# Kernel tuning notes

Measured on AMD Instinct MI355X. Metric: run time of the kernel, lower is better.

Reference implementation:

```python
import jax, jax.numpy as jnp
import numpy as np

BS, N, C_IMG, C_PT, H, W = 8, 100000, 512, 256, 48, 160


def setup_inputs() -> dict:
    key = jax.random.key(0)
    ks = jax.random.split(key, 8)
    point_feat = jax.random.normal(ks[0], (N, C_PT), dtype=jnp.float32)
    # pillar centers in LiDAR frame: x forward [10,60], y left [-10,10], z [-2,1]
    u = jax.random.uniform(ks[1], (N, 3), dtype=jnp.float32)
    pillar_centers = jnp.stack([
        10.0 + 50.0 * u[:, 0],
        -10.0 + 20.0 * u[:, 1],
        -2.0 + 3.0 * u[:, 2],
    ], axis=1)
    batch_idx = jax.random.randint(ks[2], (N,), 0, BS, dtype=jnp.int32)
    img_feat = jax.random.normal(ks[3], (BS, C_IMG, H, W), dtype=jnp.float32)
    # KITTI-style calibration (per batch, small jitter)
    f, cx, cy = 80.0, 80.0, 24.0
    P2_base = np.array([[f, 0, cx, 0], [0, f, cy, 0], [0, 0, 1, 0]], dtype=np.float32)
    Tr_base = np.array([[0, -1, 0, 0], [0, 0, -1, 0], [1, 0, 0, 0], [0, 0, 0, 1]], dtype=np.float32)
    rng = np.random.RandomState(0)
    P2 = np.stack([P2_base + 0.01 * rng.randn(3, 4).astype(np.float32) for _ in range(BS)])
    R0 = np.stack([np.eye(4, dtype=np.float32) for _ in range(BS)])
    Tr = np.stack([Tr_base + 0.001 * rng.randn(4, 4).astype(np.float32) for _ in range(BS)])
    align_w = jax.random.normal(ks[4], (C_PT, C_IMG), dtype=jnp.float32) * 0.02
    align_b = jax.random.normal(ks[5], (C_PT,), dtype=jnp.float32) * 0.02
    return {
        'point_feat': point_feat, 'pillar_centers': pillar_centers,
        'img_feat': img_feat, 'P2': jnp.asarray(P2), 'R0': jnp.asarray(R0),
        'Tr': jnp.asarray(Tr), 'align_w': align_w, 'align_b': align_b,
        'batch_idx': batch_idx, 'img_h': H, 'img_w': W,
    }


def _fuse(point_feat, pillar_centers, img_feat, P2, R0, Tr, align_w, align_b,
          batch_idx, img_h, img_w):
    n = point_feat.shape[0]
    dt = point_feat.dtype
    # --- project_to_image (vectorized over all points via per-point calib gather) ---
    pts_hom = jnp.concatenate([pillar_centers, jnp.ones((n, 1), dtype=dt)], axis=1)  # [N,4]
    pts_cam = jnp.einsum('nij,nj->ni', Tr[batch_idx], pts_hom)    # [N,4]
    pts_rect = jnp.einsum('nij,nj->ni', R0[batch_idx], pts_cam)   # [N,4]
    pts_img = jnp.einsum('nij,nj->ni', P2[batch_idx], pts_rect)   # [N,3]
    depth = jnp.clip(pts_img[:, 2:3], 1e-5, None)
    uv = pts_img[:, :2] / depth
    valid = ((pts_img[:, 2] > 0) & (uv[:, 0] >= 0) & (uv[:, 0] < img_w)
             & (uv[:, 1] >= 0) & (uv[:, 1] < img_h))
    # --- grid_sample bilinear, align_corners=True, padding_mode='zeros' ---
    # grid = 2*uv/(dim-1)-1 with align_corners=True => pixel coords == uv.
    _, C, Hf, Wf = img_feat.shape
    u_, v_ = uv[:, 0], uv[:, 1]
    x0 = jnp.floor(u_); y0 = jnp.floor(v_)
    wx1 = u_ - x0; wx0 = 1.0 - wx1
    wy1 = v_ - y0; wy0 = 1.0 - wy1

    def gather(xi, yi):
        inb = (xi >= 0) & (xi <= Wf - 1) & (yi >= 0) & (yi <= Hf - 1)
        xc = jnp.clip(xi, 0, Wf - 1).astype(jnp.int32)
        yc = jnp.clip(yi, 0, Hf - 1).astype(jnp.int32)
        f = img_feat[batch_idx, :, yc, xc]  # [N,C]
        return f * inb.astype(dt)[:, None]

    sampled = (gather(x0, y0) * (wx0 * wy0)[:, None]
               + gather(x0 + 1, y0) * (wx1 * wy0)[:, None]
               + gather(x0, y0 + 1) * (wx0 * wy1)[:, None]
               + gather(x0 + 1, y0 + 1) * (wx1 * wy1)[:, None])
    sampled = jnp.where(valid[:, None], sampled, jnp.zeros((), dtype=dt))
    # --- align (Linear) + residual add ---
    aligned = sampled @ align_w.T + align_b
    return point_feat + aligned


def reference(point_feat, pillar_centers, img_feat, P2, R0, Tr, align_w, align_b,
              batch_idx, img_h, img_w):
    return _fuse(point_feat, pillar_centers, img_feat, P2, R0, Tr,
                 align_w, align_b, batch_idx, img_h, img_w)
```

## Files before the change

### kernel.cpp

```cpp
#include <hip/hip_runtime.h>

#define C_IMG 512
#define C_PT  256
#define IMG_H 48
#define IMG_W 160
#define HWPIX (IMG_H * IMG_W)

#define MP   64
#define BK   64
#define SPAD 72

typedef short bf16x8 __attribute__((ext_vector_type(8)));
typedef float f32x4  __attribute__((ext_vector_type(4)));

static __device__ __forceinline__ unsigned short f2bf(float f) {
    unsigned u = __float_as_uint(f);
    u += 0x7fffu + ((u >> 16) & 1u);
    return (unsigned short)(u >> 16);
}
static __device__ __forceinline__ unsigned pack2(float lo, float hi) {
    return (unsigned)f2bf(lo) | ((unsigned)f2bf(hi) << 16);
}
static __device__ __forceinline__ float bflo(unsigned v) { return __uint_as_float(v << 16); }
static __device__ __forceinline__ float bfhi(unsigned v) { return __uint_as_float(v & 0xffff0000u); }

__global__ __launch_bounds__(256)
void transpose_kernel(const float* __restrict__ img, unsigned short* __restrict__ imgT) {
    __shared__ float tile[64][33];
    const int b   = blockIdx.z;
    const int hw0 = blockIdx.x * 32;
    const int c0  = blockIdx.y * 64;
    const int tx  = threadIdx.x;
    const int ty  = threadIdx.y;
    const float* src = img + (size_t)b * C_IMG * HWPIX;
    #pragma unroll
    for (int i = 0; i < 64; i += 8)
        tile[ty + i][tx] = src[(size_t)(c0 + ty + i) * HWPIX + hw0 + tx];
    __syncthreads();
    unsigned* dst = (unsigned*)(imgT + (size_t)b * HWPIX * C_IMG);
    #pragma unroll
    for (int i = 0; i < 32; i += 8) {
        const int hw = ty + i;
        dst[(size_t)(hw0 + hw) * (C_IMG / 2) + (c0 >> 1) + tx] =
            pack2(tile[2 * tx][hw], tile[2 * tx + 1][hw]);
    }
}

__global__ __launch_bounds__(256)
void cvt_w_kernel(const float* __restrict__ alw, unsigned short* __restrict__ alwT) {
    const int i = (blockIdx.x * 256 + threadIdx.x) * 8;
    const float4 a = *(const float4*)(alw + i);
    const float4 b = *(const float4*)(alw + i + 4);
    uint4 o;
    o.x = pack2(a.x, a.y); o.y = pack2(a.z, a.w);
    o.z = pack2(b.x, b.y); o.w = pack2(b.z, b.w);
    *(uint4*)(alwT + i) = o;
}

static __device__ __forceinline__ void gather_issue(
    const unsigned short* __restrict__ ib, const int* co, int cb, uint4* g)
{
    #pragma unroll
    for (int c = 0; c < 4; ++c) {
        g[2 * c]     = *(const uint4*)(ib + co[c] + cb);
        g[2 * c + 1] = *(const uint4*)(ib + co[c] + cb + 8);
    }
}
static __device__ __forceinline__ void gather_commit(
    unsigned short* __restrict__ dst, const uint4* g, const float* cw)
{
    #pragma unroll
    for (int h = 0; h < 2; ++h) {
        const unsigned* u0 = (const unsigned*)&g[0 + h];
        const unsigned* u1 = (const unsigned*)&g[2 + h];
        const unsigned* u2 = (const unsigned*)&g[4 + h];
        const unsigned* u3 = (const unsigned*)&g[6 + h];
        uint4 ov; unsigned* op = (unsigned*)&ov;
        #pragma unroll
        for (int wI = 0; wI < 4; ++wI) {
            const float vlo = cw[0]*bflo(u0[wI]) + cw[1]*bflo(u1[wI])
                            + cw[2]*bflo(u2[wI]) + cw[3]*bflo(u3[wI]);
            const float vhi = cw[0]*bfhi(u0[wI]) + cw[1]*bfhi(u1[wI])
                            + cw[2]*bfhi(u2[wI]) + cw[3]*bfhi(u3[wI]);
            op[wI] = pack2(vlo, vhi);
        }
        *(uint4*)(dst + h * 8) = ov;
    }
}

__global__ __launch_bounds__(256, 3)
void fused_trans_kernel(const float* __restrict__ pf,
                        const float* __restrict__ centers,
                        const unsigned short* __restrict__ imgT,
                        const unsigned short* __restrict__ alwT,
                        const float* __restrict__ P2,
                        const float* __restrict__ R0,
                        const float* __restrict__ Tr,
                        const float* __restrict__ alb,
                        const int*   __restrict__ bidx,
                        float* __restrict__ out,
                        int n)
{
    __shared__ float          sWg[MP][4];
    __shared__ int            sOf[MP][4];
    __shared__ unsigned short sS[2][MP][SPAD];

    const int tid = threadIdx.x;
    const int pt0 = blockIdx.x * MP;

    if (tid < MP) {
        const int p = pt0 + tid;
        float w[4] = {0.f, 0.f, 0.f, 0.f};
        int   o[4] = {0, 0, 0, 0};
        if (p < n) {
            const float cx = centers[p * 3 + 0];
            const float cy = centers[p * 3 + 1];
            const float cz = centers[p * 3 + 2];
            const int   b  = bidx[p];
            const float* tr = Tr + b * 16;
            const float c0 = tr[0]*cx + tr[1]*cy + tr[2]*cz + tr[3];
            const float c1 = tr[4]*cx + tr[5]*cy + tr[6]*cz + tr[7];
            const float c2 = tr[8]*cx + tr[9]*cy + tr[10]*cz + tr[11];
            const float c3 = tr[12]*cx + tr[13]*cy + tr[14]*cz + tr[15];
            const float* r0 = R0 + b * 16;
            const float e0 = r0[0]*c0 + r0[1]*c1 + r0[2]*c2 + r0[3]*c3;
            const float e1 = r0[4]*c0 + r0[5]*c1 + r0[6]*c2 + r0[7]*c3;
            const float e2 = r0[8]*c0 + r0[9]*c1 + r0[10]*c2 + r0[11]*c3;
            const float e3 = r0[12]*c0 + r0[13]*c1 + r0[14]*c2 + r0[15]*c3;
            const float* p2 = P2 + b * 12;
            const float ix = p2[0]*e0 + p2[1]*e1 + p2[2]*e2  + p2[3]*e3;
            const float iy = p2[4]*e0 + p2[5]*e1 + p2[6]*e2  + p2[7]*e3;
            const float iz = p2[8]*e0 + p2[9]*e1 + p2[10]*e2 + p2[11]*e3;
            const float depth = fmaxf(iz, 1e-5f);
            const float u = ix / depth;
            const float v = iy / depth;
            const bool valid = (iz > 0.f) && (u >= 0.f) && (u < (float)IMG_W)
                                         && (v >= 0.f) && (v < (float)IMG_H);
            const float x0f = floorf(u), y0f = floorf(v);
            const float wx1 = u - x0f, wx0 = 1.f - wx1;
            const float wy1 = v - y0f, wy0 = 1.f - wy1;
            const float cwv[4] = {wx0 * wy0, wx1 * wy0, wx0 * wy1, wx1 * wy1};
            #pragma unroll
            for (int j = 0; j < 4; ++j) {
                const float xf = x0f + (float)(j & 1);
                const float yf = y0f + (float)(j >> 1);
                const bool inb = (xf >= 0.f) && (xf <= (float)(IMG_W - 1))
                              && (yf >= 0.f) && (yf <= (float)(IMG_H - 1));
                const int xc = (int)fminf(fmaxf(xf, 0.f), (float)(IMG_W - 1));
                const int yc = (int)fminf(fmaxf(yf, 0.f), (float)(IMG_H - 1));
                w[j] = (valid && inb) ? cwv[j] : 0.f;
                o[j] = ((b * IMG_H + yc) * IMG_W + xc) * C_IMG;
            }
        }
        #pragma unroll
        for (int j = 0; j < 4; ++j) { sWg[tid][j] = w[j]; sOf[tid][j] = o[j]; }
    }

    f32x4 acc[4][4];
    #pragma unroll
    for (int i = 0; i < 4; ++i)
        #pragma unroll
        for (int j = 0; j < 4; ++j)
            acc[i][j] = (f32x4){0.f, 0.f, 0.f, 0.f};

    const int lane = tid & 63;
    const int wid  = tid >> 6;
    const int l15  = lane & 15;
    const int quad = lane >> 4;
    const int sp   = tid >> 2;
    const int ssub = tid & 3;

    __syncthreads();

    float cw[4]; int co[4];
    #pragma unroll
    for (int j = 0; j < 4; ++j) { cw[j] = sWg[sp][j]; co[j] = sOf[sp][j]; }
    const int cbase = ssub * 16;

    const unsigned short* bwp = alwT + (size_t)(wid * 64 + l15) * C_IMG + quad * 8;

    {
        uint4 g0[8];
        gather_issue(imgT, co, cbase, g0);
        gather_commit(&sS[0][sp][cbase], g0, cw);
    }
    __syncthreads();

    #pragma unroll
    for (int ck = 0; ck < C_IMG / BK; ++ck) {
        const int cur = ck & 1;
        uint4 gn[8];
        if (ck < C_IMG / BK - 1)
            gather_issue(imgT, co, (ck + 1) * BK + cbase, gn);

        #pragma unroll
        for (int kk = 0; kk < 2; ++kk) {
            bf16x8 bfr[4], af[4];
            #pragma unroll
            for (int nt = 0; nt < 4; ++nt)
                bfr[nt] = *(const bf16x8*)(bwp + nt * 16 * C_IMG + ck * BK + kk * 32);
            #pragma unroll
            for (int mt = 0; mt < 4; ++mt)
                af[mt] = *(const bf16x8*)&sS[cur][mt * 16 + l15][kk * 32 + quad * 8];
            #pragma unroll
            for (int mt = 0; mt < 4; ++mt)
                #pragma unroll
                for (int nt = 0; nt < 4; ++nt)
                    acc[mt][nt] = __builtin_amdgcn_mfma_f32_16x16x32_bf16(
                        af[mt], bfr[nt], acc[mt][nt], 0, 0, 0);
        }

        if (ck < C_IMG / BK - 1)
            gather_commit(&sS[cur ^ 1][sp][cbase], gn, cw);
        __syncthreads();
    }

    #pragma unroll
    for (int mt = 0; mt < 4; ++mt) {
        #pragma unroll
        for (int r = 0; r < 4; ++r) {
            const int p = pt0 + mt * 16 + quad * 4 + r;
            if (p < n) {
                #pragma unroll
                for (int nt = 0; nt < 4; ++nt) {
                    const int nc = wid * 64 + nt * 16 + l15;
                    const size_t idx = (size_t)p * C_PT + nc;
                    out[idx] = pf[idx] + alb[nc] + acc[mt][nt][r];
                }
            }
        }
    }
}

__global__ __launch_bounds__(256)
void fused_fallback_kernel(const float* __restrict__ pf,
                           const float* __restrict__ centers,
                           const float* __restrict__ img,
                           const float* __restrict__ P2,
                           const float* __restrict__ R0,
                           const float* __restrict__ Tr,
                           const float* __restrict__ alw,
                           const float* __restrict__ alb,
                           const int*   __restrict__ bidx,
                           float* __restrict__ out,
                           int n)
{
    __shared__ float          sWg[MP][4];
    __shared__ int            sOf[MP][4];
    __shared__ unsigned short sS[MP][SPAD];
    __shared__ unsigned short sW[C_PT][SPAD];

    const int tid = threadIdx.x;
    const int pt0 = blockIdx.x * MP;

    if (tid < MP) {
        const int p = pt0 + tid;
        float w[4] = {0.f, 0.f, 0.f, 0.f};
        int   o[4] = {0, 0, 0, 0};
        if (p < n) {
            const float cx = centers[p * 3 + 0];
            const float cy = centers[p * 3 + 1];
            const float cz = centers[p * 3 + 2];
            const int   b  = bidx[p];
            const float* tr = Tr + b * 16;
            const float c0 = tr[0]*cx + tr[1]*cy + tr[2]*cz + tr[3];
            const float c1 = tr[4]*cx + tr[5]*cy + tr[6]*cz + tr[7];
            const float c2 = tr[8]*cx + tr[9]*cy + tr[10]*cz + tr[11];
            const float c3 = tr[12]*cx + tr[13]*cy + tr[14]*cz + tr[15];
            const float* r0 = R0 + b * 16;
            const float e0 = r0[0]*c0 + r0[1]*c1 + r0[2]*c2 + r0[3]*c3;
            const float e1 = r0[4]*c0 + r0[5]*c1 + r0[6]*c2 + r0[7]*c3;
            const float e2 = r0[8]*c0 + r0[9]*c1 + r0[10]*c2 + r0[11]*c3;
            const float e3 = r0[12]*c0 + r0[13]*c1 + r0[14]*c2 + r0[15]*c3;
            const float* p2 = P2 + b * 12;
            const float ix = p2[0]*e0 + p2[1]*e1 + p2[2]*e2  + p2[3]*e3;
            const float iy = p2[4]*e0 + p2[5]*e1 + p2[6]*e2  + p2[7]*e3;
            const float iz = p2[8]*e0 + p2[9]*e1 + p2[10]*e2 + p2[11]*e3;
            const float depth = fmaxf(iz, 1e-5f);
            const float u = ix / depth;
            const float v = iy / depth;
            const bool valid = (iz > 0.f) && (u >= 0.f) && (u < (float)IMG_W)
                                         && (v >= 0.f) && (v < (float)IMG_H);
            const float x0f = floorf(u), y0f = floorf(v);
            const float wx1 = u - x0f, wx0 = 1.f - wx1;
            const float wy1 = v - y0f, wy0 = 1.f - wy1;
            const float cwv[4] = {wx0 * wy0, wx1 * wy0, wx0 * wy1, wx1 * wy1};
            #pragma unroll
            for (int j = 0; j < 4; ++j) {
                const float xf = x0f + (float)(j & 1);
                const float yf = y0f + (float)(j >> 1);
                const bool inb = (xf >= 0.f) && (xf <= (float)(IMG_W - 1))
                              && (yf >= 0.f) && (yf <= (float)(IMG_H - 1));
                const int xc = (int)fminf(fmaxf(xf, 0.f), (float)(IMG_W - 1));
                const int yc = (int)fminf(fmaxf(yf, 0.f), (float)(IMG_H - 1));
                w[j] = (valid && inb) ? cwv[j] : 0.f;
                o[j] = b * C_IMG * HWPIX + yc * IMG_W + xc;
            }
        }
        #pragma unroll
        for (int j = 0; j < 4; ++j) { sWg[tid][j] = w[j]; sOf[tid][j] = o[j]; }
    }

    f32x4 acc[4][4];
    #pragma unroll
    for (int i = 0; i < 4; ++i)
        #pragma unroll
        for (int j = 0; j < 4; ++j)
            acc[i][j] = (f32x4){0.f, 0.f, 0.f, 0.f};

    const int lane = tid & 63;
    const int wid  = tid >> 6;
    const int l15  = lane & 15;
    const int quad = lane >> 4;
    const int sp   = tid >> 2;
    const int ssub = tid & 3;

    __syncthreads();

    for (int ck = 0; ck < C_IMG / BK; ++ck) {
        {
            const float cw0 = sWg[sp][0], cw1 = sWg[sp][1], cw2 = sWg[sp][2], cw3 = sWg[sp][3];
            const int   co0 = sOf[sp][0], co1 = sOf[sp][1], co2 = sOf[sp][2], co3 = sOf[sp][3];
            const int   cb  = ck * BK + ssub * 16;
            const float* ib = img;
            #pragma unroll
            for (int h = 0; h < 2; ++h) {
                uint4 ov;
                unsigned* op = (unsigned*)&ov;
                #pragma unroll
                for (int wI = 0; wI < 4; ++wI) {
                    const int c = cb + h * 8 + 2 * wI;
                    const float vlo = cw0*ib[co0 + c*HWPIX] + cw1*ib[co1 + c*HWPIX]
                                    + cw2*ib[co2 + c*HWPIX] + cw3*ib[co3 + c*HWPIX];
                    const float vhi = cw0*ib[co0 + (c+1)*HWPIX] + cw1*ib[co1 + (c+1)*HWPIX]
                                    + cw2*ib[co2 + (c+1)*HWPIX] + cw3*ib[co3 + (c+1)*HWPIX];
                    op[wI] = pack2(vlo, vhi);
                }
                *(uint4*)&sS[sp][ssub * 16 + h * 8] = ov;
            }
        }
        {
            #pragma unroll
            for (int pass = 0; pass < 4; ++pass) {
                const int r = pass * 64 + (tid >> 2);
                const int c = (tid & 3) * 16;
                const float* wr = alw + (size_t)r * C_IMG + ck * BK + c;
                const float4 f0 = *(const float4*)(wr + 0);
                const float4 f1 = *(const float4*)(wr + 4);
                const float4 f2 = *(const float4*)(wr + 8);
                const float4 f3 = *(const float4*)(wr + 12);
                uint4 oa, ob;
                oa.x = pack2(f0.x, f0.y); oa.y = pack2(f0.z, f0.w);
                oa.z = pack2(f1.x, f1.y); oa.w = pack2(f1.z, f1.w);
                ob.x = pack2(f2.x, f2.y); ob.y = pack2(f2.z, f2.w);
                ob.z = pack2(f3.x, f3.y); ob.w = pack2(f3.z, f3.w);
                *(uint4*)&sW[r][c]     = oa;
                *(uint4*)&sW[r][c + 8] = ob;
            }
        }
        __syncthreads();

        #pragma unroll
        for (int kk = 0; kk < 2; ++kk) {
            bf16x8 af[4], bfr[4];
            #pragma unroll
            for (int mt = 0; mt < 4; ++mt)
                af[mt] = *(const bf16x8*)&sS[mt * 16 + l15][kk * 32 + quad * 8];
            #pragma unroll
            for (int nt = 0; nt < 4; ++nt)
                bfr[nt] = *(const bf16x8*)&sW[wid * 64 + nt * 16 + l15][kk * 32 + quad * 8];
            #pragma unroll
            for (int mt = 0; mt < 4; ++mt)
                #pragma unroll
                for (int nt = 0; nt < 4; ++nt)
                    acc[mt][nt] = __builtin_amdgcn_mfma_f32_16x16x32_bf16(
                        af[mt], bfr[nt], acc[mt][nt], 0, 0, 0);
        }
        __syncthreads();
    }

    #pragma unroll
    for (int mt = 0; mt < 4; ++mt) {
        #pragma unroll
        for (int r = 0; r < 4; ++r) {
            const int p = pt0 + mt * 16 + quad * 4 + r;
            if (p < n) {
                #pragma unroll
                for (int nt = 0; nt < 4; ++nt) {
                    const int nc = wid * 64 + nt * 16 + l15;
                    const size_t idx = (size_t)p * C_PT + nc;
                    out[idx] = pf[idx] + alb[nc] + acc[mt][nt][r];
                }
            }
        }
    }
}

extern "C" void kernel_launch(void* const* d_in, const int* in_sizes, int n_in,
                              void* d_out, int out_size, void* d_ws, size_t ws_size,
                              hipStream_t stream) {
    const float* pf      = (const float*)d_in[0];
    const float* centers = (const float*)d_in[1];
    const float* img     = (const float*)d_in[2];
    const float* P2      = (const float*)d_in[3];
    const float* R0      = (const float*)d_in[4];
    const float* Tr      = (const float*)d_in[5];
    const float* alw     = (const float*)d_in[6];
    const float* alb     = (const float*)d_in[7];
    const int*   bidx    = (const int*)d_in[8];
    float*       out     = (float*)d_out;

    const int n  = in_sizes[8];
    const int bs = in_sizes[3] / 12;
    const int nblk = (n + MP - 1) / MP;

    const size_t timg = (size_t)bs * HWPIX * C_IMG * sizeof(unsigned short);
    const size_t tw   = (size_t)C_PT * C_IMG * sizeof(unsigned short);
    if (ws_size >= timg + tw) {
        unsigned short* imgT = (unsigned short*)d_ws;
        unsigned short* alwT = (unsigned short*)((char*)d_ws + timg);
        transpose_kernel<<<dim3(HWPIX / 32, C_IMG / 64, bs), dim3(32, 8), 0, stream>>>(img, imgT);
        cvt_w_kernel<<<dim3((C_PT * C_IMG / 8) / 256), 256, 0, stream>>>(alw, alwT);
        fused_trans_kernel<<<nblk, 256, 0, stream>>>(
            pf, centers, imgT, alwT, P2, R0, Tr, alb, bidx, out, n);
    } else {
        fused_fallback_kernel<<<nblk, 256, 0, stream>>>(
            pf, centers, img, P2, R0, Tr, alw, alb, bidx, out, n);
    }
}
```

Baseline: 396.3 us.

## Project image features through linear layer before bilinear sampling

Bilinear interpolation and the linear align layer are both linear, so their order can be swapped. The weight matrix is now applied to every image pixel first (8*48*160 pixels instead of 100k points), giving a bf16 table with 256 channels per pixel. Each point then only gathers and blends four 256-channel rows and adds the residual and bias. This removes the per-point GEMM and the full-image transpose, at the cost of a dense per-pixel projection that reads the fp32 image with strided loads and writes a bf16 intermediate.

```diff
diff --git a/kernel.cpp b/kernel.cpp
--- a/kernel.cpp
+++ b/kernel.cpp
@@ -23,28 +23,6 @@
 }
 static __device__ __forceinline__ float bflo(unsigned v) { return __uint_as_float(v << 16); }
 static __device__ __forceinline__ float bfhi(unsigned v) { return __uint_as_float(v & 0xffff0000u); }
-
-__global__ __launch_bounds__(256)
-void transpose_kernel(const float* __restrict__ img, unsigned short* __restrict__ imgT) {
-    __shared__ float tile[64][33];
-    const int b   = blockIdx.z;
-    const int hw0 = blockIdx.x * 32;
-    const int c0  = blockIdx.y * 64;
-    const int tx  = threadIdx.x;
-    const int ty  = threadIdx.y;
-    const float* src = img + (size_t)b * C_IMG * HWPIX;
-    #pragma unroll
-    for (int i = 0; i < 64; i += 8)
-        tile[ty + i][tx] = src[(size_t)(c0 + ty + i) * HWPIX + hw0 + tx];
-    __syncthreads();
-    unsigned* dst = (unsigned*)(imgT + (size_t)b * HWPIX * C_IMG);
-    #pragma unroll
-    for (int i = 0; i < 32; i += 8) {
-        const int hw = ty + i;
-        dst[(size_t)(hw0 + hw) * (C_IMG / 2) + (c0 >> 1) + tx] =
-            pack2(tile[2 * tx][hw], tile[2 * tx + 1][hw]);
-    }
-}
 
 __global__ __launch_bounds__(256)
 void cvt_w_kernel(const float* __restrict__ alw, unsigned short* __restrict__ alwT) {
@@ -57,53 +35,178 @@
     *(uint4*)(alwT + i) = o;
 }
 
-static __device__ __forceinline__ void gather_issue(
-    const unsigned short* __restrict__ ib, const int* co, int cb, uint4* g)
+__global__ __launch_bounds__(256)
+void proj_kernel(const float* __restrict__ img,
+                 const unsigned short* __restrict__ wbf,
+                 unsigned short* __restrict__ PT) {
+    const int blk  = blockIdx.x;
+    const int b    = blk / (HWPIX / 64);
+    const int hw0  = (blk % (HWPIX / 64)) * 64;
+    const int tid  = threadIdx.x;
+    const int lane = tid & 63;
+    const int wid  = tid >> 6;
+    const int l15  = lane & 15;
+    const int quad = lane >> 4;
+
+    f32x4 acc[4][4];
+    #pragma unroll
+    for (int i = 0; i < 4; ++i)
+        #pragma unroll
+        for (int j = 0; j < 4; ++j)
+            acc[i][j] = (f32x4){0.f, 0.f, 0.f, 0.f};
+
+    const float* aim = img + (size_t)b * C_IMG * HWPIX + hw0 + l15;
+    const unsigned short* bw = wbf + (size_t)(wid * 64 + l15) * C_IMG + quad * 8;
+
+    for (int ck = 0; ck < C_IMG / 64; ++ck) {
+        #pragma unroll
+        for (int kk = 0; kk < 2; ++kk) {
+            const int c0 = ck * 64 + kk * 32 + quad * 8;
+            bf16x8 af[4];
+            #pragma unroll
+            for (int mt = 0; mt < 4; ++mt) {
+                const float* ap = aim + (size_t)c0 * HWPIX + mt * 16;
+                float f[8];
+                #pragma unroll
+                for (int j = 0; j < 8; ++j) f[j] = ap[j * HWPIX];
+                union { unsigned u[4]; bf16x8 v; } cv;
+                cv.u[0] = pack2(f[0], f[1]);
+                cv.u[1] = pack2(f[2], f[3]);
+                cv.u[2] = pack2(f[4], f[5]);
+                cv.u[3] = pack2(f[6], f[7]);
+                af[mt] = cv.v;
+            }
+            bf16x8 bfr[4];
+            #pragma unroll
+            for (int nt = 0; nt < 4; ++nt)
+                bfr[nt] = *(const bf16x8*)(bw + (size_t)(nt * 16) * C_IMG + ck * 64 + kk * 32);
+            #pragma unroll
+            for (int mt = 0; mt < 4; ++mt)
+                #pragma unroll
+                for (int nt = 0; nt < 4; ++nt)
+                    acc[mt][nt] = __builtin_amdgcn_mfma_f32_16x16x32_bf16(
+                        af[mt], bfr[nt], acc[mt][nt], 0, 0, 0);
+        }
+    }
+
+    #pragma unroll
+    for (int mt = 0; mt < 4; ++mt) {
+        #pragma unroll
+        for (int r = 0; r < 4; ++r) {
+            const int pix = mt * 16 + quad * 4 + r;
+            unsigned short* dst = PT + (size_t)(b * HWPIX + hw0 + pix) * C_PT;
+            #pragma unroll
+            for (int nt = 0; nt < 4; ++nt) {
+                const int nc = wid * 64 + nt * 16 + l15;
+                dst[nc] = f2bf(acc[mt][nt][r]);
+            }
+        }
+    }
+}
+
+#define PPW 4
+__global__ __launch_bounds__(256)
+void point_kernel(const float* __restrict__ pf,
+                  const float* __restrict__ centers,
+                  const unsigned short* __restrict__ PT,
+                  const float* __restrict__ P2,
+                  const float* __restrict__ R0,
+                  const float* __restrict__ Tr,
+                  const float* __restrict__ alb,
+                  const int*   __restrict__ bidx,
+                  float* __restrict__ out,
+                  int n)
 {
-    #pragma unroll
-    for (int c = 0; c < 4; ++c) {
-        g[2 * c]     = *(const uint4*)(ib + co[c] + cb);
-        g[2 * c + 1] = *(const uint4*)(ib + co[c] + cb + 8);
-    }
-}
-static __device__ __forceinline__ void gather_commit(
-    unsigned short* __restrict__ dst, const uint4* g, const float* cw)
-{
-    #pragma unroll
-    for (int h = 0; h < 2; ++h) {
-        const unsigned* u0 = (const unsigned*)&g[0 + h];
-        const unsigned* u1 = (const unsigned*)&g[2 + h];
-        const unsigned* u2 = (const unsigned*)&g[4 + h];
-        const unsigned* u3 = (const unsigned*)&g[6 + h];
-        uint4 ov; unsigned* op = (unsigned*)&ov;
-        #pragma unroll
-        for (int wI = 0; wI < 4; ++wI) {
-            const float vlo = cw[0]*bflo(u0[wI]) + cw[1]*bflo(u1[wI])
-                            + cw[2]*bflo(u2[wI]) + cw[3]*bflo(u3[wI]);
-            const float vhi = cw[0]*bfhi(u0[wI]) + cw[1]*bfhi(u1[wI])
-                            + cw[2]*bfhi(u2[wI]) + cw[3]*bfhi(u3[wI]);
-            op[wI] = pack2(vlo, vhi);
-        }
-        *(uint4*)(dst + h * 8) = ov;
-    }
-}
-
-__global__ __launch_bounds__(256, 3)
-void fused_trans_kernel(const float* __restrict__ pf,
-                        const float* __restrict__ centers,
-                        const unsigned short* __restrict__ imgT,
-                        const unsigned short* __restrict__ alwT,
-                        const float* __restrict__ P2,
-                        const float* __restrict__ R0,
-                        const float* __restrict__ Tr,
-                        const float* __restrict__ alb,
-                        const int*   __restrict__ bidx,
-                        float* __restrict__ out,
-                        int n)
+    const int tid  = threadIdx.x;
+    const int lane = tid & 63;
+    const int wid  = tid >> 6;
+    const int p0   = blockIdx.x * (4 * PPW) + wid * PPW;
+
+    const float4 ab = *(const float4*)(alb + lane * 4);
+
+    #pragma unroll
+    for (int it = 0; it < PPW; ++it) {
+        const int p = p0 + it;
+        if (p >= n) break;
+
+        const float cx = centers[p * 3 + 0];
+        const float cy = centers[p * 3 + 1];
+        const float cz = centers[p * 3 + 2];
+        const int   b  = bidx[p];
+        const float* tr = Tr + b * 16;
+        const float c0 = tr[0]*cx + tr[1]*cy + tr[2]*cz + tr[3];
+        const float c1 = tr[4]*cx + tr[5]*cy + tr[6]*cz + tr[7];
+        const float c2 = tr[8]*cx + tr[9]*cy + tr[10]*cz + tr[11];
+        const float c3 = tr[12]*cx + tr[13]*cy + tr[14]*cz + tr[15];
+        const float* r0 = R0 + b * 16;
+        const float e0 = r0[0]*c0 + r0[1]*c1 + r0[2]*c2 + r0[3]*c3;
+        const float e1 = r0[4]*c0 + r0[5]*c1 + r0[6]*c2 + r0[7]*c3;
+        const float e2 = r0[8]*c0 + r0[9]*c1 + r0[10]*c2 + r0[11]*c3;
+        const float e3 = r0[12]*c0 + r0[13]*c1 + r0[14]*c2 + r0[15]*c3;
+        const float* p2 = P2 + b * 12;
+        const float ix = p2[0]*e0 + p2[1]*e1 + p2[2]*e2  + p2[3]*e3;
+        const float iy = p2[4]*e0 + p2[5]*e1 + p2[6]*e2  + p2[7]*e3;
+        const float iz = p2[8]*e0 + p2[9]*e1 + p2[10]*e2 + p2[11]*e3;
+        const float depth = fmaxf(iz, 1e-5f);
+        const float u = ix / depth;
+        const float v = iy / depth;
+        const bool valid = (iz > 0.f) && (u >= 0.f) && (u < (float)IMG_W)
+                                     && (v >= 0.f) && (v < (float)IMG_H);
+        const float x0f = floorf(u), y0f = floorf(v);
+        const float wx1 = u - x0f, wx0 = 1.f - wx1;
+        const float wy1 = v - y0f, wy0 = 1.f - wy1;
+        const float cwv[4] = {wx0 * wy0, wx1 * wy0, wx0 * wy1, wx1 * wy1};
+        float wgt[4]; int off[4];
+        #pragma unroll
+        for (int j = 0; j < 4; ++j) {
+            const float xf = x0f + (float)(j & 1);
+            const float yf = y0f + (float)(j >> 1);
+            const bool inb = (xf >= 0.f) && (xf <= (float)(IMG_W - 1))
+                          && (yf >= 0.f) && (yf <= (float)(IMG_H - 1));
+            const int xc = (int)fminf(fmaxf(xf, 0.f), (float)(IMG_W - 1));
+            const int yc = (int)fminf(fmaxf(yf, 0.f), (float)(IMG_H - 1));
+            wgt[j] = (valid && inb) ? cwv[j] : 0.f;
+            off[j] = ((b * IMG_H + yc) * IMG_W + xc) * C_PT;
+        }
+
+        float s0 = 0.f, s1 = 0.f, s2 = 0.f, s3 = 0.f;
+        #pragma unroll
+        for (int j = 0; j < 4; ++j) {
+            const uint2 g = *(const uint2*)(PT + off[j] + lane * 4);
+            s0 = fmaf(wgt[j], bflo(g.x), s0);
+            s1 = fmaf(wgt[j], bfhi(g.x), s1);
+            s2 = fmaf(wgt[j], bflo(g.y), s2);
+            s3 = fmaf(wgt[j], bfhi(g.y), s3);
+        }
+
+        const size_t idx = (size_t)p * C_PT + lane * 4;
+        const float4 pv = *(const float4*)(pf + idx);
+        float4 ov;
+        ov.x = pv.x + ab.x + s0;
+        ov.y = pv.y + ab.y + s1;
+        ov.z = pv.z + ab.z + s2;
+        ov.w = pv.w + ab.w + s3;
+        *(float4*)(out + idx) = ov;
+    }
+}
+
+__global__ __launch_bounds__(256)
+void fused_fallback_kernel(const float* __restrict__ pf,
+                           const float* __restrict__ centers,
+                           const float* __restrict__ img,
+                           const float* __restrict__ P2,
+                           const float* __restrict__ R0,
+                           const float* __restrict__ Tr,
+                           const float* __restrict__ alw,
+                           const float* __restrict__ alb,
+                           const int*   __restrict__ bidx,
+                           float* __restrict__ out,
+                           int n)
 {
     __shared__ float          sWg[MP][4];
     __shared__ int            sOf[MP][4];
-    __shared__ unsigned short sS[2][MP][SPAD];
+    __shared__ unsigned short sS[MP][SPAD];
+    __shared__ unsigned short sW[C_PT][SPAD];
 
     const int tid = threadIdx.x;
     const int pt0 = blockIdx.x * MP;
@@ -149,151 +252,6 @@
                 const int xc = (int)fminf(fmaxf(xf, 0.f), (float)(IMG_W - 1));
                 const int yc = (int)fminf(fmaxf(yf, 0.f), (float)(IMG_H - 1));
                 w[j] = (valid && inb) ? cwv[j] : 0.f;
-                o[j] = ((b * IMG_H + yc) * IMG_W + xc) * C_IMG;
-            }
-        }
-        #pragma unroll
-        for (int j = 0; j < 4; ++j) { sWg[tid][j] = w[j]; sOf[tid][j] = o[j]; }
-    }
-
-    f32x4 acc[4][4];
-    #pragma unroll
-    for (int i = 0; i < 4; ++i)
-        #pragma unroll
-        for (int j = 0; j < 4; ++j)
-            acc[i][j] = (f32x4){0.f, 0.f, 0.f, 0.f};
-
-    const int lane = tid & 63;
-    const int wid  = tid >> 6;
-    const int l15  = lane & 15;
-    const int quad = lane >> 4;
-    const int sp   = tid >> 2;
-    const int ssub = tid & 3;
-
-    __syncthreads();
-
-    float cw[4]; int co[4];
-    #pragma unroll
-    for (int j = 0; j < 4; ++j) { cw[j] = sWg[sp][j]; co[j] = sOf[sp][j]; }
-    const int cbase = ssub * 16;
-
-    const unsigned short* bwp = alwT + (size_t)(wid * 64 + l15) * C_IMG + quad * 8;
-
-    {
-        uint4 g0[8];
-        gather_issue(imgT, co, cbase, g0);
-        gather_commit(&sS[0][sp][cbase], g0, cw);
-    }
-    __syncthreads();
-
-    #pragma unroll
-    for (int ck = 0; ck < C_IMG / BK; ++ck) {
-        const int cur = ck & 1;
-        uint4 gn[8];
-        if (ck < C_IMG / BK - 1)
-            gather_issue(imgT, co, (ck + 1) * BK + cbase, gn);
-
-        #pragma unroll
-        for (int kk = 0; kk < 2; ++kk) {
-            bf16x8 bfr[4], af[4];
-            #pragma unroll
-            for (int nt = 0; nt < 4; ++nt)
-                bfr[nt] = *(const bf16x8*)(bwp + nt * 16 * C_IMG + ck * BK + kk * 32);
-            #pragma unroll
-            for (int mt = 0; mt < 4; ++mt)
-                af[mt] = *(const bf16x8*)&sS[cur][mt * 16 + l15][kk * 32 + quad * 8];
-            #pragma unroll
-            for (int mt = 0; mt < 4; ++mt)
-                #pragma unroll
-                for (int nt = 0; nt < 4; ++nt)
-                    acc[mt][nt] = __builtin_amdgcn_mfma_f32_16x16x32_bf16(
-                        af[mt], bfr[nt], acc[mt][nt], 0, 0, 0);
-        }
-
-        if (ck < C_IMG / BK - 1)
-            gather_commit(&sS[cur ^ 1][sp][cbase], gn, cw);
-        __syncthreads();
-    }
-
-    #pragma unroll
-    for (int mt = 0; mt < 4; ++mt) {
-        #pragma unroll
-        for (int r = 0; r < 4; ++r) {
-            const int p = pt0 + mt * 16 + quad * 4 + r;
-            if (p < n) {
-                #pragma unroll
-                for (int nt = 0; nt < 4; ++nt) {
-                    const int nc = wid * 64 + nt * 16 + l15;
-                    const size_t idx = (size_t)p * C_PT + nc;
-                    out[idx] = pf[idx] + alb[nc] + acc[mt][nt][r];
-                }
-            }
-        }
-    }
-}
-
-__global__ __launch_bounds__(256)
-void fused_fallback_kernel(const float* __restrict__ pf,
-                           const float* __restrict__ centers,
-                           const float* __restrict__ img,
-                           const float* __restrict__ P2,
-                           const float* __restrict__ R0,
-                           const float* __restrict__ Tr,
-                           const float* __restrict__ alw,
-                           const float* __restrict__ alb,
-                           const int*   __restrict__ bidx,
-                           float* __restrict__ out,
-                           int n)
-{
-    __shared__ float          sWg[MP][4];
-    __shared__ int            sOf[MP][4];
-    __shared__ unsigned short sS[MP][SPAD];
-    __shared__ unsigned short sW[C_PT][SPAD];
-
-    const int tid = threadIdx.x;
-    const int pt0 = blockIdx.x * MP;
-
-    if (tid < MP) {
-        const int p = pt0 + tid;
-        float w[4] = {0.f, 0.f, 0.f, 0.f};
-        int   o[4] = {0, 0, 0, 0};
-        if (p < n) {
-            const float cx = centers[p * 3 + 0];
-            const float cy = centers[p * 3 + 1];
-            const float cz = centers[p * 3 + 2];
-            const int   b  = bidx[p];
-            const float* tr = Tr + b * 16;
-            const float c0 = tr[0]*cx + tr[1]*cy + tr[2]*cz + tr[3];
-            const float c1 = tr[4]*cx + tr[5]*cy + tr[6]*cz + tr[7];
-            const float c2 = tr[8]*cx + tr[9]*cy + tr[10]*cz + tr[11];
-            const float c3 = tr[12]*cx + tr[13]*cy + tr[14]*cz + tr[15];
-            const float* r0 = R0 + b * 16;
-            const float e0 = r0[0]*c0 + r0[1]*c1 + r0[2]*c2 + r0[3]*c3;
-            const float e1 = r0[4]*c0 + r0[5]*c1 + r0[6]*c2 + r0[7]*c3;
-            const float e2 = r0[8]*c0 + r0[9]*c1 + r0[10]*c2 + r0[11]*c3;
-            const float e3 = r0[12]*c0 + r0[13]*c1 + r0[14]*c2 + r0[15]*c3;
-            const float* p2 = P2 + b * 12;
-            const float ix = p2[0]*e0 + p2[1]*e1 + p2[2]*e2  + p2[3]*e3;
-            const float iy = p2[4]*e0 + p2[5]*e1 + p2[6]*e2  + p2[7]*e3;
-            const float iz = p2[8]*e0 + p2[9]*e1 + p2[10]*e2 + p2[11]*e3;
-            const float depth = fmaxf(iz, 1e-5f);
-            const float u = ix / depth;
-            const float v = iy / depth;
-            const bool valid = (iz > 0.f) && (u >= 0.f) && (u < (float)IMG_W)
-                                         && (v >= 0.f) && (v < (float)IMG_H);
-            const float x0f = floorf(u), y0f = floorf(v);
-            const float wx1 = u - x0f, wx0 = 1.f - wx1;
-            const float wy1 = v - y0f, wy0 = 1.f - wy1;
-            const float cwv[4] = {wx0 * wy0, wx1 * wy0, wx0 * wy1, wx1 * wy1};
-            #pragma unroll
-            for (int j = 0; j < 4; ++j) {
-                const float xf = x0f + (float)(j & 1);
-                const float yf = y0f + (float)(j >> 1);
-                const bool inb = (xf >= 0.f) && (xf <= (float)(IMG_W - 1))
-                              && (yf >= 0.f) && (yf <= (float)(IMG_H - 1));
-                const int xc = (int)fminf(fmaxf(xf, 0.f), (float)(IMG_W - 1));
-                const int yc = (int)fminf(fmaxf(yf, 0.f), (float)(IMG_H - 1));
-                w[j] = (valid && inb) ? cwv[j] : 0.f;
                 o[j] = b * C_IMG * HWPIX + yc * IMG_W + xc;
             }
         }
@@ -412,18 +370,18 @@
 
     const int n  = in_sizes[8];
     const int bs = in_sizes[3] / 12;
-    const int nblk = (n + MP - 1) / MP;
-
-    const size_t timg = (size_t)bs * HWPIX * C_IMG * sizeof(unsigned short);
-    const size_t tw   = (size_t)C_PT * C_IMG * sizeof(unsigned short);
-    if (ws_size >= timg + tw) {
-        unsigned short* imgT = (unsigned short*)d_ws;
-        unsigned short* alwT = (unsigned short*)((char*)d_ws + timg);
-        transpose_kernel<<<dim3(HWPIX / 32, C_IMG / 64, bs), dim3(32, 8), 0, stream>>>(img, imgT);
-        cvt_w_kernel<<<dim3((C_PT * C_IMG / 8) / 256), 256, 0, stream>>>(alw, alwT);
-        fused_trans_kernel<<<nblk, 256, 0, stream>>>(
-            pf, centers, imgT, alwT, P2, R0, Tr, alb, bidx, out, n);
+
+    const size_t tpt = (size_t)bs * HWPIX * C_PT * sizeof(unsigned short);
+    const size_t tw  = (size_t)C_PT * C_IMG * sizeof(unsigned short);
+    if (ws_size >= tpt + tw) {
+        unsigned short* PT  = (unsigned short*)d_ws;
+        unsigned short* wbf = (unsigned short*)((char*)d_ws + tpt);
+        cvt_w_kernel<<<(C_PT * C_IMG / 8) / 256, 256, 0, stream>>>(alw, wbf);
+        proj_kernel<<<bs * (HWPIX / 64), 256, 0, stream>>>(img, wbf, PT);
+        point_kernel<<<(n + 4 * PPW * 4 - 1) / (4 * PPW * 4) * 4, 256, 0, stream>>>(
+            pf, centers, PT, P2, R0, Tr, alb, bidx, out, n);
     } else {
+        const int nblk = (n + MP - 1) / MP;
         fused_fallback_kernel<<<nblk, 256, 0, stream>>>(
             pf, centers, img, P2, R0, Tr, alw, alb, bidx, out, n);
     }
```

New measurement: 386.5 us. 1.03x faster.
